# Optimization experiments

Measured on AMD Instinct MI355X. Metric: run time of the kernel, lower is better.

## Reference

```python
import jax, jax.numpy as jnp
import numpy as np

V_NUM = 50000
E_NUM = 10000
EMB_DIM = 128
LAYER_NUM = 2
N_INC = 600000
VE_TAU = 1.0
EV_TAU = 1.0


def _segment_softmax(a, idx, num_segments):
    # a: [N, 1], idx: [N] -> softmax within each segment (stable)
    m = jax.ops.segment_max(a, idx, num_segments=num_segments)
    ex = jnp.exp(a - m[idx])
    s = jax.ops.segment_sum(ex, idx, num_segments=num_segments)
    return ex / s[idx]


def setup_inputs() -> dict:
    key = jax.random.key(0)
    ks = jax.random.split(key, 12)
    std = (2.0 ** 0.5) * (2.0 / (EMB_DIM + 1)) ** 0.5  # xavier_normal gain sqrt(2)
    v_emb = jax.random.normal(ks[0], (V_NUM, EMB_DIM), dtype=jnp.float32)
    t_emb = jax.random.normal(ks[1], (V_NUM, EMB_DIM), dtype=jnp.float32)
    e_emb = jax.random.normal(ks[2], (E_NUM, EMB_DIM), dtype=jnp.float32)
    v_idx = jax.random.randint(ks[3], (N_INC, 1), 0, V_NUM)
    e_idx = jax.random.randint(ks[4], (N_INC, 1), 0, E_NUM)
    ve = jnp.concatenate([v_idx, e_idx], axis=1).astype(jnp.int32)
    p = lambda k: std * jax.random.normal(k, (LAYER_NUM, EMB_DIM), dtype=jnp.float32)
    return {
        "v_emb": v_emb, "t_emb": t_emb, "e_emb": e_emb, "ve": ve,
        "av_v2e": p(ks[5]), "at_v2e": p(ks[6]), "ae_v2e": p(ks[7]),
        "av_e2v": p(ks[8]), "at_e2v": p(ks[9]), "ae_e2v": p(ks[10]),
    }


def _agg(v_fea, t_fea, e_fea, v, e, av, at, ae, tau, dst_idx, dst_num, src_fea, src_idx):
    # attention logits per incidence: tanh(a_v[v] + a_t[v] + a_e[e]) / tau, shape [N, 1]
    sv = v_fea @ av[:, None]  # [V,1]
    st = t_fea @ at[:, None]  # [V,1]
    se = e_fea @ ae[:, None]  # [E,1]
    a = jnp.tanh(sv[v] + st[v] + se[e]) / tau
    a = _segment_softmax(a, dst_idx, dst_num)
    return jax.ops.segment_sum(a * src_fea[src_idx], dst_idx, num_segments=dst_num)


def reference(v_emb, t_emb, e_emb, ve, av_v2e, at_v2e, ae_v2e, av_e2v, at_e2v, ae_e2v):
    v = ve[:, 0]
    e = ve[:, 1]
    v_stack = [v_emb]
    e_stack = [e_emb]
    for l in range(LAYER_NUM):
        v_fea = v_stack[-1]
        e_fea = e_stack[-1]
        # V2E: softmax over edge segments, aggregate node features into edges
        e_new = _agg(v_fea, t_emb, e_fea, v, e, av_v2e[l], at_v2e[l], ae_v2e[l],
                     VE_TAU, e, E_NUM, v_fea, v)
        e_stack.append(jax.nn.relu(e_new))
        # E2V uses pre-relu e_new (as in original: e_fea_ not reassigned to relu)
        v_new = _agg(v_fea, t_emb, e_new, v, e, av_e2v[l], at_e2v[l], ae_e2v[l],
                     EV_TAU, v, V_NUM, e_new, e)
        v_stack.append(jax.nn.relu(v_new))
    v_out = jnp.mean(jnp.stack(v_stack, axis=1), axis=1)
    e_out = jnp.mean(jnp.stack(e_stack, axis=1), axis=1)
    return (v_out, e_out)
```

## Files before the change

### kernel.cpp

```cpp
#include <hip/hip_runtime.h>

#define DIM 128
#define VSTRIDE 48
#define ESTRIDE 128
#define BUILD_BLOCKS 512
#define NXCD 8

typedef unsigned short ushort_t;
typedef unsigned int   uint_t;

__device__ inline ushort_t f2bf(float f) {
    uint_t u = __float_as_uint(f);
    u += 0x7FFF + ((u >> 16) & 1);
    return (ushort_t)(u >> 16);
}
__device__ inline float bf2f(ushort_t h) { return __uint_as_float((uint_t)h << 16); }
__device__ inline float lo16(uint_t u) { return bf2f((ushort_t)u); }
__device__ inline float hi16(uint_t u) { return bf2f((ushort_t)(u >> 16)); }

__device__ inline float wfun(float x) {
    float t = __expf(2.f * x);
    float r = __builtin_amdgcn_rcpf(t + 1.f);
    return __expf(1.f - 2.f * r);
}

__device__ inline float wred(float x) {
    #pragma unroll
    for (int o = 32; o; o >>= 1) x += __shfl_xor(x, o, 64);
    return x;
}

__global__ void k_setup(const int2* __restrict__ ve, int N,
                        int* __restrict__ cntV, int* __restrict__ cntE,
                        ushort_t* __restrict__ bV, ushort_t* __restrict__ bE,
                        const float* __restrict__ v_emb, const float* __restrict__ t_emb,
                        const float* __restrict__ e_emb,
                        const float* __restrict__ av0, const float* __restrict__ at0,
                        const float* __restrict__ av1, const float* __restrict__ at1,
                        const float* __restrict__ at2, const float* __restrict__ at3,
                        const float* __restrict__ ae0,
                        uint_t* __restrict__ vb,
                        float* __restrict__ scv0, float* __restrict__ scv1,
                        float* __restrict__ st2, float* __restrict__ st3,
                        float* __restrict__ sce0,
                        int V, int E, int gVpre)
{
    int b = blockIdx.x;
    if (b < BUILD_BLOCKS) {
        const int g = b & (NXCD - 1);
        const int j = b >> 3;
        const int nj = BUILD_BLOCKS / NXCD;
        int k0 = (int)((size_t)N * j / nj), k1 = (int)((size_t)N * (j + 1) / nj);
        int vlo = (int)((size_t)V * g / NXCD), vhi = (int)((size_t)V * (g + 1) / NXCD);
        int elo = (int)((size_t)E * g / NXCD), ehi = (int)((size_t)E * (g + 1) / NXCD);
        for (int k = k0 + threadIdx.x; k < k1; k += 256) {
            int2 p = ve[k];
            if (p.x >= vlo && p.x < vhi) {
                int s = atomicAdd(&cntV[p.x], 1);
                if (s < VSTRIDE) bV[(size_t)p.x * VSTRIDE + s] = (ushort_t)p.y;
            }
            if (p.y >= elo && p.y < ehi) {
                int s = atomicAdd(&cntE[p.y], 1);
                if (s < ESTRIDE) bE[(size_t)p.y * ESTRIDE + s] = (ushort_t)p.x;
            }
        }
        return;
    }
    b -= BUILD_BLOCKS;
    int lane = threadIdx.x & 63;
    int wv   = threadIdx.x >> 6;
    if (b < gVpre) {
        int row = b * 4 + wv;
        if (row >= V) return;
        float2 v = ((const float2*)(v_emb + (size_t)row * DIM))[lane];
        float2 t = ((const float2*)(t_emb + (size_t)row * DIM))[lane];
        vb[(size_t)row * 64 + lane] = (uint_t)f2bf(v.x) | ((uint_t)f2bf(v.y) << 16);
        float2 a0 = ((const float2*)av0)[lane], b0 = ((const float2*)at0)[lane];
        float2 a1 = ((const float2*)av1)[lane], b1 = ((const float2*)at1)[lane];
        float2 b2 = ((const float2*)at2)[lane], b3 = ((const float2*)at3)[lane];
        float d0 = v.x * a0.x + v.y * a0.y + t.x * b0.x + t.y * b0.y;
        float d1 = v.x * a1.x + v.y * a1.y + t.x * b1.x + t.y * b1.y;
        float d2 = t.x * b2.x + t.y * b2.y;
        float d3 = t.x * b3.x + t.y * b3.y;
        d0 = wred(d0); d1 = wred(d1); d2 = wred(d2); d3 = wred(d3);
        if (lane == 0) { scv0[row] = d0; scv1[row] = d1; st2[row] = d2; st3[row] = d3; }
    } else {
        int row = (b - gVpre) * 4 + wv;
        if (row >= E) return;
        float2 v = ((const float2*)(e_emb + (size_t)row * DIM))[lane];
        float2 a = ((const float2*)ae0)[lane];
        float d = wred(v.x * a.x + v.y * a.y);
        if (lane == 0) sce0[row] = d;
    }
}

__global__ void k_gatherE(const ushort_t* __restrict__ bucket, const int* __restrict__ cnt,
                          const float* __restrict__ scSrc, const float* __restrict__ scDst,
                          const uint_t* __restrict__ src_bf,
                          float* __restrict__ outF, uint_t* __restrict__ outB, int reluB,
                          const float* __restrict__ pd0, float* __restrict__ osc0,
                          const float* __restrict__ pd1, float* __restrict__ osc1, int relu1,
                          const float* __restrict__ meanA, const float* __restrict__ meanB,
                          int ndst)
{
    __shared__ float l2[4][64][2];
    __shared__ float lw[4];
    int dst = blockIdx.x;
    if (dst >= ndst) return;
    int wv = threadIdx.x >> 6, lane = threadIdx.x & 63;
    int m = cnt[dst]; if (m > ESTRIDE) m = ESTRIDE;
    const ushort_t* s = bucket + (size_t)dst * ESTRIDE;
    float sd = scDst[dst];
    int m4 = (m + 3) >> 2;
    int j0 = wv * m4;
    int cw = min(m, j0 + m4) - j0;
    int   idxl = 0;
    float wl   = 0.f;
    if (lane < cw) {
        idxl = s[j0 + lane];
        wl   = wfun(scSrc[idxl] + sd);
    }
    float ws = wred(wl);
    float a0 = 0.f, a1 = 0.f;
    int j = 0;
    for (; j + 4 <= cw; j += 4) {
        int   i0 = __shfl(idxl, j, 64),     i1 = __shfl(idxl, j + 1, 64);
        int   i2 = __shfl(idxl, j + 2, 64), i3 = __shfl(idxl, j + 3, 64);
        float w0 = __shfl(wl, j, 64),       w1 = __shfl(wl, j + 1, 64);
        float w2 = __shfl(wl, j + 2, 64),   w3 = __shfl(wl, j + 3, 64);
        uint_t u0 = src_bf[(size_t)i0 * 64 + lane];
        uint_t u1 = src_bf[(size_t)i1 * 64 + lane];
        uint_t u2 = src_bf[(size_t)i2 * 64 + lane];
        uint_t u3 = src_bf[(size_t)i3 * 64 + lane];
        a0 += w0 * lo16(u0) + w1 * lo16(u1) + w2 * lo16(u2) + w3 * lo16(u3);
        a1 += w0 * hi16(u0) + w1 * hi16(u1) + w2 * hi16(u2) + w3 * hi16(u3);
    }
    for (; j < cw; ++j) {
        int   i0 = __shfl(idxl, j, 64);
        float w0 = __shfl(wl, j, 64);
        uint_t u0 = src_bf[(size_t)i0 * 64 + lane];
        a0 += w0 * lo16(u0); a1 += w0 * hi16(u0);
    }
    l2[wv][lane][0] = a0; l2[wv][lane][1] = a1;
    if (lane == 0) lw[wv] = ws;
    __syncthreads();
    if (wv != 0) return;
    a0 = l2[0][lane][0] + l2[1][lane][0] + l2[2][lane][0] + l2[3][lane][0];
    a1 = l2[0][lane][1] + l2[1][lane][1] + l2[2][lane][1] + l2[3][lane][1];
    ws = lw[0] + lw[1] + lw[2] + lw[3];
    float inv = (ws > 0.f) ? 1.f / ws : 0.f;
    float rx = a0 * inv, ry = a1 * inv;
    if (outB) {
        float bx = reluB ? fmaxf(rx, 0.f) : rx;
        float by = reluB ? fmaxf(ry, 0.f) : ry;
        outB[(size_t)dst * 64 + lane] = (uint_t)f2bf(bx) | ((uint_t)f2bf(by) << 16);
    }
    if (pd0) {
        float2 q = ((const float2*)pd0)[lane];
        float d = wred(rx * q.x + ry * q.y);
        if (lane == 0) osc0[dst] = d;
    }
    if (pd1) {
        float x0 = relu1 ? fmaxf(rx, 0.f) : rx;
        float x1 = relu1 ? fmaxf(ry, 0.f) : ry;
        float2 q = ((const float2*)pd1)[lane];
        float d = wred(x0 * q.x + x1 * q.y);
        if (lane == 0) osc1[dst] = d;
    }
    float2 r; r.x = rx; r.y = ry;
    if (meanA) {
        float2 ma = ((const float2*)(meanA + (size_t)dst * DIM))[lane];
        float2 mb = ((const float2*)(meanB + (size_t)dst * DIM))[lane];
        r.x = (ma.x + fmaxf(mb.x, 0.f) + fmaxf(rx, 0.f)) * (1.f / 3.f);
        r.y = (ma.y + fmaxf(mb.y, 0.f) + fmaxf(ry, 0.f)) * (1.f / 3.f);
    }
    ((float2*)(outF + (size_t)dst * DIM))[lane] = r;
}

__global__ void k_gatherV(const ushort_t* __restrict__ bucket, const int* __restrict__ cnt,
                          const float* __restrict__ scSrc, const float* __restrict__ scDst,
                          const uint_t* __restrict__ src_bf,
                          float* __restrict__ outF, uint_t* __restrict__ outB, int reluB,
                          const float* __restrict__ pd0, const float* __restrict__ sta0,
                          float* __restrict__ osc0, int relu0,
                          const float* __restrict__ pd1, const float* __restrict__ sta1,
                          float* __restrict__ osc1, int relu1,
                          const float* __restrict__ meanA, const float* __restrict__ meanB,
                          int ndst)
{
    int dst  = blockIdx.x * 4 + (threadIdx.x >> 6);
    int lane = threadIdx.x & 63;
    if (dst >= ndst) return;
    int m = cnt[dst]; if (m > VSTRIDE) m = VSTRIDE;
    const ushort_t* s = bucket + (size_t)dst * VSTRIDE;
    float sd = scDst[dst];
    int   idxl = 0;
    float wl   = 0.f;
    if (lane < m) {
        idxl = s[lane];
        wl   = wfun(scSrc[idxl] + sd);
    }
    float ws = wred(wl);
    float a0 = 0.f, a1 = 0.f;
    int j = 0;
    for (; j + 4 <= m; j += 4) {
        int   i0 = __shfl(idxl, j, 64),     i1 = __shfl(idxl, j + 1, 64);
        int   i2 = __shfl(idxl, j + 2, 64), i3 = __shfl(idxl, j + 3, 64);
        float w0 = __shfl(wl, j, 64),       w1 = __shfl(wl, j + 1, 64);
        float w2 = __shfl(wl, j + 2, 64),   w3 = __shfl(wl, j + 3, 64);
        uint_t u0 = src_bf[(size_t)i0 * 64 + lane];
        uint_t u1 = src_bf[(size_t)i1 * 64 + lane];
        uint_t u2 = src_bf[(size_t)i2 * 64 + lane];
        uint_t u3 = src_bf[(size_t)i3 * 64 + lane];
        a0 += w0 * lo16(u0) + w1 * lo16(u1) + w2 * lo16(u2) + w3 * lo16(u3);
        a1 += w0 * hi16(u0) + w1 * hi16(u1) + w2 * hi16(u2) + w3 * hi16(u3);
    }
    for (; j < m; ++j) {
        int   i0 = __shfl(idxl, j, 64);
        float w0 = __shfl(wl, j, 64);
        uint_t u0 = src_bf[(size_t)i0 * 64 + lane];
        a0 += w0 * lo16(u0); a1 += w0 * hi16(u0);
    }
    float inv = (ws > 0.f) ? 1.f / ws : 0.f;
    float rx = a0 * inv, ry = a1 * inv;
    if (outB) {
        float bx = reluB ? fmaxf(rx, 0.f) : rx;
        float by = reluB ? fmaxf(ry, 0.f) : ry;
        outB[(size_t)dst * 64 + lane] = (uint_t)f2bf(bx) | ((uint_t)f2bf(by) << 16);
    }
    if (pd0) {
        float x0 = relu0 ? fmaxf(rx, 0.f) : rx;
        float x1 = relu0 ? fmaxf(ry, 0.f) : ry;
        float2 q = ((const float2*)pd0)[lane];
        float d = wred(x0 * q.x + x1 * q.y);
        if (lane == 0) osc0[dst] = d + (sta0 ? sta0[dst] : 0.f);
    }
    if (pd1) {
        float x0 = relu1 ? fmaxf(rx, 0.f) : rx;
        float x1 = relu1 ? fmaxf(ry, 0.f) : ry;
        float2 q = ((const float2*)pd1)[lane];
        float d = wred(x0 * q.x + x1 * q.y);
        if (lane == 0) osc1[dst] = d + (sta1 ? sta1[dst] : 0.f);
    }
    float2 r; r.x = rx; r.y = ry;
    if (meanA) {
        float2 ma = ((const float2*)(meanA + (size_t)dst * DIM))[lane];
        float2 mb = ((const float2*)(meanB + (size_t)dst * DIM))[lane];
        r.x = (ma.x + fmaxf(mb.x, 0.f) + fmaxf(rx, 0.f)) * (1.f / 3.f);
        r.y = (ma.y + fmaxf(mb.y, 0.f) + fmaxf(ry, 0.f)) * (1.f / 3.f);
    }
    ((float2*)(outF + (size_t)dst * DIM))[lane] = r;
}

extern "C" void kernel_launch(void* const* d_in, const int* in_sizes, int n_in,
                              void* d_out, int out_size, void* d_ws, size_t ws_size,
                              hipStream_t stream)
{
    const float* v_emb  = (const float*)d_in[0];
    const float* t_emb  = (const float*)d_in[1];
    const float* e_emb  = (const float*)d_in[2];
    const int2*  ve     = (const int2*)d_in[3];
    const float* av_v2e = (const float*)d_in[4];
    const float* at_v2e = (const float*)d_in[5];
    const float* ae_v2e = (const float*)d_in[6];
    const float* av_e2v = (const float*)d_in[7];
    const float* at_e2v = (const float*)d_in[8];
    const float* ae_e2v = (const float*)d_in[9];

    const int V = in_sizes[0] / DIM;
    const int E = in_sizes[2] / DIM;
    const int N = in_sizes[3] / 2;

    char* p = (char*)d_ws;
    auto alloc = [&](size_t bytes) { char* r = p; p += (bytes + 255) & ~(size_t)255; return r; };
    float* v_new0 = (float*)alloc((size_t)V * DIM * 4);
    float* e_new0 = (float*)alloc((size_t)E * DIM * 4);
    uint_t* vb    = (uint_t*)alloc((size_t)V * 64 * 4);
    uint_t* eb    = (uint_t*)alloc((size_t)E * 64 * 4);
    ushort_t* bV  = (ushort_t*)alloc((size_t)V * VSTRIDE * 2);
    ushort_t* bE  = (ushort_t*)alloc((size_t)E * ESTRIDE * 2);
    int*   cntV   = (int*)alloc((size_t)(V + E) * 4);
    int*   cntE   = cntV + V;
    float* scv0   = (float*)alloc((size_t)V * 4);
    float* scv1   = (float*)alloc((size_t)V * 4);
    float* scv2   = (float*)alloc((size_t)V * 4);
    float* scv3   = (float*)alloc((size_t)V * 4);
    float* st2    = (float*)alloc((size_t)V * 4);
    float* st3    = (float*)alloc((size_t)V * 4);
    float* sce0   = (float*)alloc((size_t)E * 4);
    float* sce1   = (float*)alloc((size_t)E * 4);
    float* sce2   = (float*)alloc((size_t)E * 4);
    float* sce3   = (float*)alloc((size_t)E * 4);

    float* out_v = (float*)d_out;
    float* out_e = out_v + (size_t)V * DIM;

    hipMemsetAsync(cntV, 0, (size_t)(V + E) * 4, stream);

    const int gVpre = (V + 3) / 4, gEpre = (E + 3) / 4;
    k_setup<<<BUILD_BLOCKS + gVpre + gEpre, 256, 0, stream>>>(
        ve, N, cntV, cntE, bV, bE,
        v_emb, t_emb, e_emb,
        av_v2e, at_v2e, av_e2v, at_e2v, at_v2e + DIM, at_e2v + DIM, ae_v2e,
        vb, scv0, scv1, st2, st3, sce0, V, E, gVpre);

    k_gatherE<<<E, 256, 0, stream>>>(bE, cntE, scv0, sce0, vb,
        e_new0, eb, 0, ae_e2v, sce1, ae_v2e + DIM, sce2, 1,
        nullptr, nullptr, E);

    k_gatherV<<<(V + 3) / 4, 256, 0, stream>>>(bV, cntV, sce1, scv1, eb,
        v_new0, vb, 1,
        av_v2e + DIM, st2, scv2, 1,
        av_e2v + DIM, st3, scv3, 1,
        nullptr, nullptr, V);

    k_gatherE<<<E, 256, 0, stream>>>(bE, cntE, scv2, sce2, vb,
        out_e, eb, 0, ae_e2v + DIM, sce3, nullptr, nullptr, 0,
        e_emb, e_new0, E);

    k_gatherV<<<(V + 3) / 4, 256, 0, stream>>>(bV, cntV, sce3, scv3, eb,
        out_v, nullptr, 0,
        nullptr, nullptr, nullptr, 0,
        nullptr, nullptr, nullptr, 0,
        v_emb, v_new0, V);
}
```

Baseline: 198.0 us.

## Build adjacency buckets via two-pass slice partition with LDS-local scatter

Replaces the global-atomic scatter that built per-node and per-edge incidence buckets with a two-stage scheme. A new partition kernel histograms incidences into 128 coarse slices per side and scatters packed (local id, neighbor) words into per-slice staging arrays. Each setup block then builds its slice's buckets in shared memory with LDS atomics and writes them out contiguously. This trades scattered global atomics and writes for an extra kernel launch and staging traffic. Fixed slice capacities (CAPS) silently drop entries if a slice overflows, and the new ordering within buckets is nondeterministic.

```diff
diff --git a/kernel.cpp b/kernel.cpp
--- a/kernel.cpp
+++ b/kernel.cpp
@@ -3,8 +3,10 @@
 #define DIM 128
 #define VSTRIDE 48
 #define ESTRIDE 128
-#define BUILD_BLOCKS 512
-#define NXCD 8
+#define NSL 128
+#define DSLE 79
+#define DSLV 391
+#define CAPS 5440
 
 typedef unsigned short ushort_t;
 typedef unsigned int   uint_t;
@@ -30,9 +32,46 @@
     return x;
 }
 
-__global__ void k_setup(const int2* __restrict__ ve, int N,
-                        int* __restrict__ cntV, int* __restrict__ cntE,
-                        ushort_t* __restrict__ bV, ushort_t* __restrict__ bE,
+__global__ void k_part(const int2* __restrict__ ve, int N,
+                       int* __restrict__ curE, int* __restrict__ curV,
+                       uint_t* __restrict__ peE, uint_t* __restrict__ peV)
+{
+    __shared__ int hE[NSL], hV[NSL], baE[NSL], baV[NSL];
+    int k0 = blockIdx.x * 1024;
+    int k1 = min(N, k0 + 1024);
+    if (threadIdx.x < NSL) { hE[threadIdx.x] = 0; }
+    else if (threadIdx.x < 2 * NSL) { hV[threadIdx.x - NSL] = 0; }
+    __syncthreads();
+    for (int k = k0 + threadIdx.x; k < k1; k += 256) {
+        int2 p = ve[k];
+        atomicAdd(&hE[(uint_t)p.y / DSLE], 1);
+        atomicAdd(&hV[(uint_t)p.x / DSLV], 1);
+    }
+    __syncthreads();
+    if (threadIdx.x < NSL) {
+        int t = threadIdx.x;
+        baE[t] = atomicAdd(&curE[t], hE[t]); hE[t] = 0;
+    } else if (threadIdx.x < 2 * NSL) {
+        int t = threadIdx.x - NSL;
+        baV[t] = atomicAdd(&curV[t], hV[t]); hV[t] = 0;
+    }
+    __syncthreads();
+    for (int k = k0 + threadIdx.x; k < k1; k += 256) {
+        int2 p = ve[k];
+        uint_t sE = (uint_t)p.y / DSLE, sV = (uint_t)p.x / DSLV;
+        int rE = baE[sE] + atomicAdd(&hE[sE], 1);
+        if (rE < CAPS)
+            peE[(size_t)sE * CAPS + rE] = ((uint_t)(p.y - sE * DSLE) << 16) | (uint_t)p.x;
+        int rV = baV[sV] + atomicAdd(&hV[sV], 1);
+        if (rV < CAPS)
+            peV[(size_t)sV * CAPS + rV] = ((uint_t)(p.x - sV * DSLV) << 16) | (uint_t)p.y;
+    }
+}
+
+__global__ void k_setup(const uint_t* __restrict__ peE, const uint_t* __restrict__ peV,
+                        const int* __restrict__ curE, const int* __restrict__ curV,
+                        int* __restrict__ cntE, int* __restrict__ cntV,
+                        ushort_t* __restrict__ bE, ushort_t* __restrict__ bV,
                         const float* __restrict__ v_emb, const float* __restrict__ t_emb,
                         const float* __restrict__ e_emb,
                         const float* __restrict__ av0, const float* __restrict__ at0,
@@ -45,28 +84,37 @@
                         float* __restrict__ sce0,
                         int V, int E, int gVpre)
 {
+    __shared__ __align__(16) ushort_t sb[DSLV * VSTRIDE];
+    __shared__ int shc[DSLV];
     int b = blockIdx.x;
-    if (b < BUILD_BLOCKS) {
-        const int g = b & (NXCD - 1);
-        const int j = b >> 3;
-        const int nj = BUILD_BLOCKS / NXCD;
-        int k0 = (int)((size_t)N * j / nj), k1 = (int)((size_t)N * (j + 1) / nj);
-        int vlo = (int)((size_t)V * g / NXCD), vhi = (int)((size_t)V * (g + 1) / NXCD);
-        int elo = (int)((size_t)E * g / NXCD), ehi = (int)((size_t)E * (g + 1) / NXCD);
-        for (int k = k0 + threadIdx.x; k < k1; k += 256) {
-            int2 p = ve[k];
-            if (p.x >= vlo && p.x < vhi) {
-                int s = atomicAdd(&cntV[p.x], 1);
-                if (s < VSTRIDE) bV[(size_t)p.x * VSTRIDE + s] = (ushort_t)p.y;
-            }
-            if (p.y >= elo && p.y < ehi) {
-                int s = atomicAdd(&cntE[p.y], 1);
-                if (s < ESTRIDE) bE[(size_t)p.y * ESTRIDE + s] = (ushort_t)p.x;
-            }
+    if (b < 2 * NSL) {
+        int isV = (b >= NSL);
+        int s = isV ? b - NSL : b;
+        int dsl = isV ? DSLV : DSLE;
+        int stride = isV ? VSTRIDE : ESTRIDE;
+        int lo = s * dsl;
+        int nd = min((isV ? V : E) - lo, dsl);
+        if (nd <= 0) return;
+        const uint_t* pe = (isV ? peV : peE) + (size_t)s * CAPS;
+        int len = (isV ? curV : curE)[s]; if (len > CAPS) len = CAPS;
+        for (int t = threadIdx.x; t < nd; t += 256) shc[t] = 0;
+        __syncthreads();
+        for (int i = threadIdx.x; i < len; i += 256) {
+            uint_t u = pe[i];
+            int dl = (int)(u >> 16);
+            int slot = atomicAdd(&shc[dl], 1);
+            if (slot < stride) sb[dl * stride + slot] = (ushort_t)(u & 0xffffu);
         }
+        __syncthreads();
+        int* cnt = isV ? cntV : cntE;
+        for (int t = threadIdx.x; t < nd; t += 256) cnt[lo + t] = shc[t];
+        uint_t* gout = (uint_t*)((isV ? bV : bE) + (size_t)lo * stride);
+        const uint_t* lsrc = (const uint_t*)sb;
+        int nu = nd * stride / 2;
+        for (int t = threadIdx.x; t < nu; t += 256) gout[t] = lsrc[t];
         return;
     }
-    b -= BUILD_BLOCKS;
+    b -= 2 * NSL;
     int lane = threadIdx.x & 63;
     int wv   = threadIdx.x >> 6;
     if (b < gVpre) {
@@ -279,8 +327,12 @@
     uint_t* eb    = (uint_t*)alloc((size_t)E * 64 * 4);
     ushort_t* bV  = (ushort_t*)alloc((size_t)V * VSTRIDE * 2);
     ushort_t* bE  = (ushort_t*)alloc((size_t)E * ESTRIDE * 2);
-    int*   cntV   = (int*)alloc((size_t)(V + E) * 4);
+    uint_t* peE   = (uint_t*)alloc((size_t)NSL * CAPS * 4);
+    uint_t* peV   = (uint_t*)alloc((size_t)NSL * CAPS * 4);
+    int*   cntV   = (int*)alloc((size_t)(V + E + 2 * NSL) * 4);
     int*   cntE   = cntV + V;
+    int*   curE   = cntE + E;
+    int*   curV   = curE + NSL;
     float* scv0   = (float*)alloc((size_t)V * 4);
     float* scv1   = (float*)alloc((size_t)V * 4);
     float* scv2   = (float*)alloc((size_t)V * 4);
@@ -295,11 +347,13 @@
     float* out_v = (float*)d_out;
     float* out_e = out_v + (size_t)V * DIM;
 
-    hipMemsetAsync(cntV, 0, (size_t)(V + E) * 4, stream);
+    hipMemsetAsync(curE, 0, (size_t)2 * NSL * 4, stream);
+
+    k_part<<<(N + 1023) / 1024, 256, 0, stream>>>(ve, N, curE, curV, peE, peV);
 
     const int gVpre = (V + 3) / 4, gEpre = (E + 3) / 4;
-    k_setup<<<BUILD_BLOCKS + gVpre + gEpre, 256, 0, stream>>>(
-        ve, N, cntV, cntE, bV, bE,
+    k_setup<<<2 * NSL + gVpre + gEpre, 256, 0, stream>>>(
+        peE, peV, curE, curV, cntE, cntV, bE, bV,
         v_emb, t_emb, e_emb,
         av_v2e, at_v2e, av_e2v, at_e2v, at_v2e + DIM, at_e2v + DIM, ae_v2e,
         vb, scv0, scv1, st2, st3, sce0, V, E, gVpre);
```

Result: faster. 174.3 us (-12.0%).
